# Optimization experiments

Measured on AMD Instinct MI355X. Metric: run time of the kernel, lower is better.

The kernel has to match this reference:

```python
import jax, jax.numpy as jnp
import numpy as np

B, T, D_IN, D_H, D_P = 256, 512, 256, 512, 512

def _lin(k, out_d, in_d):
    # torch nn.Linear default init: U(-1/sqrt(in_d), 1/sqrt(in_d))
    k1, k2 = jax.random.split(k)
    bound = 1.0 / np.sqrt(in_d)
    W = jax.random.uniform(k1, (out_d, in_d), jnp.float32, -bound, bound)
    b = jax.random.uniform(k2, (out_d,), jnp.float32, -bound, bound)
    return W, b

def setup_inputs() -> dict:
    key = jax.random.key(0)
    ks = jax.random.split(key, 8)
    x = jax.random.normal(ks[0], (B, T, D_IN), jnp.float32)
    # RNNCell params (torch init: U(-1/sqrt(hidden), 1/sqrt(hidden)) for all)
    bh = 1.0 / np.sqrt(D_H)
    k = jax.random.split(ks[1], 4)
    W_ih = jax.random.uniform(k[0], (D_H, D_IN), jnp.float32, -bh, bh)
    b_ih = jax.random.uniform(k[1], (D_H,), jnp.float32, -bh, bh)
    W_hh = jax.random.uniform(k[2], (D_H, D_H), jnp.float32, -bh, bh)
    b_hh = jax.random.uniform(k[3], (D_H,), jnp.float32, -bh, bh)
    W_ip, b_ip = _lin(ks[2], D_P, D_IN)
    W_hp, b_hp = _lin(ks[3], D_P, D_H)
    W_g, b_g = _lin(ks[4], D_P, D_IN + D_H)
    W_r, b_r = _lin(ks[5], D_P, D_P)
    W_o, b_o = _lin(ks[6], D_P, D_P)
    return dict(x=x, W_ih=W_ih, b_ih=b_ih, W_hh=W_hh, b_hh=b_hh,
                W_ip=W_ip, b_ip=b_ip, W_hp=W_hp, b_hp=b_hp,
                W_g=W_g, b_g=b_g, W_r=W_r, b_r=b_r, W_o=W_o, b_o=b_o)

def reference(x, W_ih, b_ih, W_hh, b_hh, W_ip, b_ip, W_hp, b_hp,
              W_g, b_g, W_r, b_r, W_o, b_o):
    batch = x.shape[0]
    # Precompute time-parallel projections of x outside the recurrence.
    x_ih = jnp.einsum('bti,hi->bth', x, W_ih) + b_ih + b_hh   # RNN input term
    x_proj_all = jnp.einsum('bti,pi->btp', x, W_ip) + b_ip
    # gate = sigmoid([x_t, h] @ W_g^T + b_g); split W_g into x-part and h-part
    W_gx, W_gh = W_g[:, :x.shape[-1]], W_g[:, x.shape[-1]:]
    gate_x_all = jnp.einsum('bti,pi->btp', x, W_gx) + b_g

    h0 = jnp.zeros((batch, W_hh.shape[0]), x.dtype)

    def step(h, inputs):
        x_ih_t, x_proj, gate_x = inputs
        h = jnp.tanh(x_ih_t + h @ W_hh.T)                # RNNCell (b_ih+b_hh folded in)
        h_proj = h @ W_hp.T + b_hp
        gate = jax.nn.sigmoid(gate_x + h @ W_gh.T)
        blended = gate * h_proj + (1.0 - gate) * x_proj
        res = blended @ W_r.T + b_r
        out_t = jax.nn.relu(res + blended)
        out_t = out_t @ W_o.T + b_o
        return h, out_t

    xs = (jnp.swapaxes(x_ih, 0, 1),       # (T, B, H)
          jnp.swapaxes(x_proj_all, 0, 1), # (T, B, P)
          jnp.swapaxes(gate_x_all, 0, 1)) # (T, B, P)
    _, outs = jax.lax.scan(step, h0, xs)
    return jnp.swapaxes(outs, 0, 1)       # (B, T, P)
```

## Files before the change

kernel.cpp:

```cpp
#include <hip/hip_runtime.h>
#include <hip/hip_bf16.h>
#include <cstdint>

#define RB   256
#define RT   512
#define ROWS (RB*RT)

typedef __attribute__((ext_vector_type(8))) short bf16x8;
typedef __attribute__((ext_vector_type(4))) short s16x4;
typedef __attribute__((ext_vector_type(4))) float f32x4;

#define DEV static __device__ __forceinline__

DEV float bf2f(unsigned short u){
  union { unsigned int i; float f; } v; v.i = ((unsigned int)u) << 16; return v.f;
}
DEV float blo(unsigned int u){
  union { unsigned int i; float f; } v; v.i = u << 16; return v.f;
}
DEV float bhi(unsigned int u){
  union { unsigned int i; float f; } v; v.i = u & 0xffff0000u; return v.f;
}
DEV unsigned short f2bf(float f){
  union { float f; unsigned int i; } v; v.f = f;
  unsigned int x = v.i;
  return (unsigned short)((x + 0x7fffu + ((x >> 16) & 1u)) >> 16);
}
DEV unsigned int cvt_pk_bf16(float lo, float hi){
  unsigned int r;
  asm("v_cvt_pk_bf16_f32 %0, %1, %2" : "=v"(r) : "v"(lo), "v"(hi));
  return r;
}
DEV float tanh_fast(float x){
  float e  = __expf(2.f * x);
  return 1.f - 2.f * __builtin_amdgcn_rcpf(e + 1.f);
}
DEV float sigmoid_fast(float x){
  float xc = fminf(fmaxf(x, -30.f), 30.f);
  return __builtin_amdgcn_rcpf(1.f + __expf(-xc));
}
DEV void gl_lds16(const void* g, void* l){
  __builtin_amdgcn_global_load_lds(
      (const __attribute__((address_space(1))) unsigned int*)g,
      (__attribute__((address_space(3))) unsigned int*)l, 16, 0, 0);
}

struct ConvArgs {
  const float* src[15];
  unsigned short* dst[15];
  long pre[16];
};

__global__ __launch_bounds__(256) void conv_k(ConvArgs a, long total)
{
  long stride = (long)gridDim.x * blockDim.x;
  for (long idx = (long)blockIdx.x * blockDim.x + threadIdx.x; idx < total; idx += stride){
    int t = 0;
    #pragma unroll
    for (int j = 0; j < 14; j++) t += (idx >= a.pre[j + 1]) ? 1 : 0;
    long local = idx - a.pre[t];
    float4 v = ((const float4*)a.src[t])[local];
    s16x4 o;
    o[0] = (short)f2bf(v.x); o[1] = (short)f2bf(v.y);
    o[2] = (short)f2bf(v.z); o[3] = (short)f2bf(v.w);
    ((s16x4*)a.dst[t])[local] = o;
  }
}

__global__ __launch_bounds__(256, 2) void gemm_k(
    const unsigned short* __restrict__ A, int lda,
    const unsigned short* __restrict__ W, int ldb,
    const unsigned short* __restrict__ bias,
    const unsigned short* __restrict__ bias2,
    const unsigned short* __restrict__ addsrc,
    void* __restrict__ C,
    int K, int act, int out_f32)
{
  __shared__ unsigned short As[128*64];
  __shared__ unsigned short Bs[128*64];
  const int tid = threadIdx.x, w = tid >> 6, l = tid & 63;
  const int wm = w >> 1, wn = w & 1;
  const int lr = l & 15, lk = (l >> 4) * 8;
  const long row0 = (long)blockIdx.x * 128;
  const int  col0 = blockIdx.y * 128;

  f32x4 acc[4][4] = {};

  for (int k0 = 0; k0 < K; k0 += 64){
    __syncthreads();
    #pragma unroll
    for (int i = 0; i < 4; i++){
      int chunk = i*256 + tid;
      int r = chunk >> 3, kc = (chunk & 7) * 8;
      gl_lds16(A + (row0 + r)*lda + k0 + kc, (unsigned short*)As + (i*256 + w*64)*8);
      gl_lds16(W + (long)(col0 + r)*ldb + k0 + kc, (unsigned short*)Bs + (i*256 + w*64)*8);
    }
    asm volatile("s_waitcnt vmcnt(0)" ::: "memory");
    __syncthreads();
    #pragma unroll
    for (int ks = 0; ks < 2; ks++){
      bf16x8 a[4], b[4];
      #pragma unroll
      for (int mt = 0; mt < 4; mt++) a[mt] = *(const bf16x8*)&As[(wm*64 + mt*16 + lr)*64 + ks*32 + lk];
      #pragma unroll
      for (int nt = 0; nt < 4; nt++) b[nt] = *(const bf16x8*)&Bs[(wn*64 + nt*16 + lr)*64 + ks*32 + lk];
      #pragma unroll
      for (int mt = 0; mt < 4; mt++)
        #pragma unroll
        for (int nt = 0; nt < 4; nt++)
          acc[mt][nt] = __builtin_amdgcn_mfma_f32_16x16x32_bf16(a[mt], b[nt], acc[mt][nt], 0, 0, 0);
    }
  }

  #pragma unroll
  for (int nt = 0; nt < 4; nt++){
    int c = col0 + wn*64 + nt*16 + lr;
    float bv = bf2f(bias[c]);
    if (bias2) bv += bf2f(bias2[c]);
    #pragma unroll
    for (int mt = 0; mt < 4; mt++){
      #pragma unroll
      for (int i = 0; i < 4; i++){
        long r = row0 + wm*64 + mt*16 + (l >> 4)*4 + i;
        float v = acc[mt][nt][i] + bv;
        if (addsrc) v += bf2f(addsrc[r*512 + c]);
        if (act) v = fmaxf(v, 0.f);
        if (out_f32) ((float*)C)[r*512 + c] = v;
        else ((unsigned short*)C)[r*512 + c] = f2bf(v);
      }
    }
  }
}

__global__ __launch_bounds__(512, 2) void recur_k(
    const unsigned short* __restrict__ xih,
    const unsigned short* __restrict__ Whh,
    unsigned short* __restrict__ H)
{
  extern __shared__ unsigned short lds[];
  unsigned short* Wl = lds;
  unsigned short* hb = lds + 512*136;

  const int tid = threadIdx.x, w = tid >> 6, l = tid & 63;
  const int lr = l & 15, hi = l >> 4, lk = hi * 8;
  const int b0 = blockIdx.x * 16;
  const int cbase = w * 64;

  #pragma unroll
  for (int i = 0; i < 16; i++){
    int id = i*512 + tid;
    int c = id >> 4, j = (id & 15) * 8;
    *(bf16x8*)&Wl[c*136 + j] = *(const bf16x8*)&Whh[c*512 + 384 + j];
  }
  for (int i = tid; i < 16*520; i += 512) hb[i] = 0;

  bf16x8 wa[4][12];
  #pragma unroll
  for (int nt = 0; nt < 4; nt++){
    const unsigned short* wp = Whh + (cbase + nt*16 + lr)*512 + lk;
    #pragma unroll
    for (int ks = 0; ks < 12; ks++)
      wa[nt][ks] = *(const bf16x8*)&wp[ks*32];
  }
  #pragma unroll
  for (int nt = 0; nt < 4; nt++)
    #pragma unroll
    for (int ks = 0; ks < 12; ks++)
      asm volatile("" : "+v"(wa[nt][ks]));

  __syncthreads();

  const unsigned short* hrd = &hb[lr*520 + lk];
  const unsigned short* wlb = &Wl[(cbase + lr)*136 + lk];
  unsigned short*       hwr = &hb[lr*520 + cbase + hi*4];

  const long xbase = ((long)(b0 + lr) * RT) * 512 + cbase + hi*4;
  const unsigned short* xr = xih + xbase;
  unsigned short*       hr = H   + xbase;

  #pragma unroll 1
  for (int t = 0; t < RT; t++){
    uint2 xu[4];
    #pragma unroll
    for (int nt = 0; nt < 4; nt++)
      xu[nt] = *(const uint2*)(xr + nt*16);

    f32x4 acc[4] = {};
    #pragma unroll
    for (int ks = 0; ks < 12; ks++){
      bf16x8 hf = *(const bf16x8*)(hrd + ks*32);
      #pragma unroll
      for (int nt = 0; nt < 4; nt++)
        acc[nt] = __builtin_amdgcn_mfma_f32_16x16x32_bf16(wa[nt][ks], hf, acc[nt], 0, 0, 0);
    }
    #pragma unroll
    for (int ks = 0; ks < 4; ks++){
      bf16x8 hf = *(const bf16x8*)(hrd + (12 + ks)*32);
      #pragma unroll
      for (int nt = 0; nt < 4; nt++){
        bf16x8 af = *(const bf16x8*)(wlb + (nt*16)*136 + ks*32);
        acc[nt] = __builtin_amdgcn_mfma_f32_16x16x32_bf16(af, hf, acc[nt], 0, 0, 0);
      }
    }

    uint2 P[4];
    #pragma unroll
    for (int nt = 0; nt < 4; nt++){
      float v0 = tanh_fast(acc[nt][0] + blo(xu[nt].x));
      float v1 = tanh_fast(acc[nt][1] + bhi(xu[nt].x));
      float v2 = tanh_fast(acc[nt][2] + blo(xu[nt].y));
      float v3 = tanh_fast(acc[nt][3] + bhi(xu[nt].y));
      P[nt].x = cvt_pk_bf16(v0, v1);
      P[nt].y = cvt_pk_bf16(v2, v3);
    }

    #pragma unroll
    for (int nt = 0; nt < 4; nt++)
      *(uint2*)(hr + nt*16) = P[nt];

    __syncthreads();
    #pragma unroll
    for (int nt = 0; nt < 4; nt++)
      *(uint2*)(hwr + nt*16) = P[nt];
    __syncthreads();

    xr += 512; hr += 512;
  }
}

__global__ __launch_bounds__(256, 2) void blend_k(
    const unsigned short* __restrict__ X,
    const unsigned short* __restrict__ Hm,
    const unsigned short* __restrict__ Wg,
    const unsigned short* __restrict__ Wip,
    const unsigned short* __restrict__ Whp,
    const unsigned short* __restrict__ bg,
    const unsigned short* __restrict__ bip,
    const unsigned short* __restrict__ bhp,
    unsigned short* __restrict__ Out)
{
  __shared__ unsigned short As[128*64];
  __shared__ unsigned short Gs[128*64];
  __shared__ unsigned short Ps[128*64];
  const int tid = threadIdx.x, w = tid >> 6, l = tid & 63;
  const int wm = w >> 1, wn = w & 1;
  const int lr = l & 15, lk = (l >> 4) * 8;
  const long row0 = (long)blockIdx.x * 128;
  const int  col0 = blockIdx.y * 128;

  f32x4 accg[4][4] = {}, accp[4][4] = {};
  unsigned int xpp[4][4][2];

  #pragma unroll 1
  for (int k0 = 0; k0 < 768; k0 += 64){
    const bool ph1 = (k0 < 256);
    __syncthreads();
    #pragma unroll
    for (int i = 0; i < 4; i++){
      int chunk = i*256 + tid;
      int r = chunk >> 3, kc = (chunk & 7) * 8;
      const unsigned short* asrc = ph1 ? (X  + (row0 + r)*256 + k0 + kc)
                                       : (Hm + (row0 + r)*512 + (k0 - 256) + kc);
      gl_lds16(asrc, (unsigned short*)As + (i*256 + w*64)*8);
      gl_lds16(Wg + (long)(col0 + r)*768 + k0 + kc, (unsigned short*)Gs + (i*256 + w*64)*8);
      const unsigned short* psrc = ph1 ? (Wip + (col0 + r)*256 + k0 + kc)
                                       : (Whp + (col0 + r)*512 + (k0 - 256) + kc);
      gl_lds16(psrc, (unsigned short*)Ps + (i*256 + w*64)*8);
    }
    asm volatile("s_waitcnt vmcnt(0)" ::: "memory");
    __syncthreads();
    #pragma unroll
    for (int ks = 0; ks < 2; ks++){
      bf16x8 a[4], gq[4], pq[4];
      #pragma unroll
      for (int mt = 0; mt < 4; mt++) a[mt]  = *(const bf16x8*)&As[(wm*64 + mt*16 + lr)*64 + ks*32 + lk];
      #pragma unroll
      for (int nt = 0; nt < 4; nt++){
        gq[nt] = *(const bf16x8*)&Gs[(wn*64 + nt*16 + lr)*64 + ks*32 + lk];
        pq[nt] = *(const bf16x8*)&Ps[(wn*64 + nt*16 + lr)*64 + ks*32 + lk];
      }
      #pragma unroll
      for (int mt = 0; mt < 4; mt++)
        #pragma unroll
        for (int nt = 0; nt < 4; nt++){
          accg[mt][nt] = __builtin_amdgcn_mfma_f32_16x16x32_bf16(a[mt], gq[nt], accg[mt][nt], 0, 0, 0);
          accp[mt][nt] = __builtin_amdgcn_mfma_f32_16x16x32_bf16(a[mt], pq[nt], accp[mt][nt], 0, 0, 0);
        }
    }
    if (k0 == 192){
      #pragma unroll
      for (int mt = 0; mt < 4; mt++)
        #pragma unroll
        for (int nt = 0; nt < 4; nt++){
          xpp[mt][nt][0] = (unsigned)f2bf(accp[mt][nt][0]) | ((unsigned)f2bf(accp[mt][nt][1]) << 16);
          xpp[mt][nt][1] = (unsigned)f2bf(accp[mt][nt][2]) | ((unsigned)f2bf(accp[mt][nt][3]) << 16);
          accp[mt][nt] = (f32x4){0.f, 0.f, 0.f, 0.f};
        }
    }
  }

  #pragma unroll
  for (int nt = 0; nt < 4; nt++){
    int c = col0 + wn*64 + nt*16 + lr;
    float bgv = bf2f(bg[c]), bipv = bf2f(bip[c]), bhpv = bf2f(bhp[c]);
    #pragma unroll
    for (int mt = 0; mt < 4; mt++){
      #pragma unroll
      for (int i = 0; i < 4; i++){
        long r = row0 + wm*64 + mt*16 + (l >> 4)*4 + i;
        float g  = sigmoid_fast(accg[mt][nt][i] + bgv);
        float hp = accp[mt][nt][i] + bhpv;
        unsigned u = xpp[mt][nt][i >> 1];
        float xp = bf2f((unsigned short)((i & 1) ? (u >> 16) : (u & 0xffff))) + bipv;
        float v = g * hp + (1.f - g) * xp;
        Out[r*512 + c] = f2bf(v);
      }
    }
  }
}

extern "C" void kernel_launch(void* const* d_in, const int* in_sizes, int n_in,
                              void* d_out, int out_size, void* d_ws, size_t ws_size,
                              hipStream_t stream)
{
  static const long nelem[15] = {
    (long)ROWS*256,
    512*256, 512,
    512*512, 512,
    512*256, 512,
    512*512, 512,
    512*768, 512,
    512*512, 512,
    512*512, 512
  };

  unsigned char* ob = (unsigned char*)d_out;
  unsigned char* wb = (unsigned char*)d_ws;
  ConvArgs ca;
  long pre = 0;
  size_t doff = 0;
  for (int i = 0; i < 15; i++){
    ca.src[i] = (const float*)d_in[i];
    if (i == 13)      ca.dst[i] = (unsigned short*)(wb + 134217728u);
    else if (i == 14) ca.dst[i] = (unsigned short*)(wb + 134742016u);
    else              ca.dst[i] = (unsigned short*)(ob + doff);
    ca.pre[i] = pre;
    pre += nelem[i] / 4;
    if (i == 0) doff = 67108864u;
    else if (i < 13) doff += (size_t)nelem[i] * 2;
  }
  ca.pre[15] = pre;
  const long total_chunks = pre;

  const unsigned short* xb  = ca.dst[0];
  const unsigned short* Wih = ca.dst[1];
  const unsigned short* bih = ca.dst[2];
  const unsigned short* Whh = ca.dst[3];
  const unsigned short* bhh = ca.dst[4];
  const unsigned short* Wip = ca.dst[5];
  const unsigned short* bip = ca.dst[6];
  const unsigned short* Whp = ca.dst[7];
  const unsigned short* bhp = ca.dst[8];
  const unsigned short* Wg  = ca.dst[9];
  const unsigned short* bg  = ca.dst[10];
  const unsigned short* Wr  = ca.dst[11];
  const unsigned short* br  = ca.dst[12];
  const unsigned short* Wo  = ca.dst[13];
  const unsigned short* bo  = ca.dst[14];

  unsigned short* xih  = (unsigned short*)(ob + 75497472u);
  unsigned short* wsb  = (unsigned short*)d_ws;

  dim3 grid(ROWS / 128, 4), block(256);

  conv_k<<<2048, 256, 0, stream>>>(ca, total_chunks);

  gemm_k<<<grid, block, 0, stream>>>(xb, 256, Wih, 256, bih, bhh, nullptr, xih, 256, 0, 0);

  static const int kRecurLds = 512*136*2 + 16*520*2;
  hipFuncSetAttribute((const void*)recur_k, hipFuncAttributeMaxDynamicSharedMemorySize, kRecurLds);
  recur_k<<<16, 512, kRecurLds, stream>>>(xih, Whh, wsb);

  blend_k<<<grid, block, 0, stream>>>(xb, wsb, Wg, Wip, Whp, bg, bip, bhp, xih);

  gemm_k<<<grid, block, 0, stream>>>(xih, 512, Wr, 512, br, nullptr, xih, wsb, 512, 1, 0);

  gemm_k<<<grid, block, 0, stream>>>(wsb, 512, Wo, 512, bo, nullptr, nullptr, d_out, 512, 0, 1);
}
```

Measured before the change: 2.103 ms.

## Double-buffer GEMM loads and restructure recurrence W_hh split across registers, LDS, global

```diff
diff --git a/kernel.cpp b/kernel.cpp
--- a/kernel.cpp
+++ b/kernel.cpp
@@ -9,6 +9,8 @@
 typedef __attribute__((ext_vector_type(8))) short bf16x8;
 typedef __attribute__((ext_vector_type(4))) short s16x4;
 typedef __attribute__((ext_vector_type(4))) float f32x4;
+typedef __attribute__((ext_vector_type(4))) int   i32x4;
+typedef unsigned long long ull;
 
 #define DEV static __device__ __forceinline__
 
@@ -65,6 +67,17 @@
     o[2] = (short)f2bf(v.z); o[3] = (short)f2bf(v.w);
     ((s16x4*)a.dst[t])[local] = o;
   }
+}
+
+__global__ __launch_bounds__(256) void wtail_k(
+    const unsigned short* __restrict__ Whh, unsigned short* __restrict__ Wt)
+{
+  int id = blockIdx.x * 256 + threadIdx.x;
+  int fi = id >> 6, l = id & 63;
+  int w  = fi >> 4, si = (fi >> 2) & 3, nt = fi & 3;
+  int row = w*64 + nt*16 + (l & 15);
+  int col = (12 + si)*32 + (l >> 4)*8;
+  *(bf16x8*)&Wt[(long)id * 8] = *(const bf16x8*)&Whh[row*512 + col];
 }
 
 __global__ __launch_bounds__(256, 2) void gemm_k(
@@ -76,8 +89,8 @@
     void* __restrict__ C,
     int K, int act, int out_f32)
 {
-  __shared__ unsigned short As[128*64];
-  __shared__ unsigned short Bs[128*64];
+  __shared__ unsigned short As[2][128*64];
+  __shared__ unsigned short Bs[2][128*64];
   const int tid = threadIdx.x, w = tid >> 6, l = tid & 63;
   const int wm = w >> 1, wn = w & 1;
   const int lr = l & 15, lk = (l >> 4) * 8;
@@ -86,31 +99,45 @@
 
   f32x4 acc[4][4] = {};
 
-  for (int k0 = 0; k0 < K; k0 += 64){
-    __syncthreads();
-    #pragma unroll
-    for (int i = 0; i < 4; i++){
-      int chunk = i*256 + tid;
-      int r = chunk >> 3, kc = (chunk & 7) * 8;
-      gl_lds16(A + (row0 + r)*lda + k0 + kc, (unsigned short*)As + (i*256 + w*64)*8);
-      gl_lds16(W + (long)(col0 + r)*ldb + k0 + kc, (unsigned short*)Bs + (i*256 + w*64)*8);
-    }
-    asm volatile("s_waitcnt vmcnt(0)" ::: "memory");
-    __syncthreads();
+#define GSTAGE(buf, kk) { \
+    _Pragma("unroll") \
+    for (int i = 0; i < 4; i++){ \
+      int chunk = i*256 + tid; \
+      int r = chunk >> 3, kc = (chunk & 7) * 8; \
+      gl_lds16(A + (row0 + r)*lda + (kk) + kc, (unsigned short*)As[buf] + (i*256 + w*64)*8); \
+      gl_lds16(W + (long)(col0 + r)*ldb + (kk) + kc, (unsigned short*)Bs[buf] + (i*256 + w*64)*8); \
+    } }
+
+  GSTAGE(0, 0)
+  const int nst = K >> 6;
+  for (int s = 0; s < nst; s++){
+    const int cb = s & 1;
+    if (s + 1 < nst){
+      GSTAGE(cb ^ 1, (s + 1) * 64)
+      asm volatile("s_waitcnt vmcnt(8)" ::: "memory");
+    } else {
+      asm volatile("s_waitcnt vmcnt(0)" ::: "memory");
+    }
+    __builtin_amdgcn_s_barrier();
+    asm volatile("" ::: "memory");
     #pragma unroll
     for (int ks = 0; ks < 2; ks++){
       bf16x8 a[4], b[4];
       #pragma unroll
-      for (int mt = 0; mt < 4; mt++) a[mt] = *(const bf16x8*)&As[(wm*64 + mt*16 + lr)*64 + ks*32 + lk];
-      #pragma unroll
-      for (int nt = 0; nt < 4; nt++) b[nt] = *(const bf16x8*)&Bs[(wn*64 + nt*16 + lr)*64 + ks*32 + lk];
+      for (int mt = 0; mt < 4; mt++) a[mt] = *(const bf16x8*)&As[cb][(wm*64 + mt*16 + lr)*64 + ks*32 + lk];
+      #pragma unroll
+      for (int nt = 0; nt < 4; nt++) b[nt] = *(const bf16x8*)&Bs[cb][(wn*64 + nt*16 + lr)*64 + ks*32 + lk];
       #pragma unroll
       for (int mt = 0; mt < 4; mt++)
         #pragma unroll
         for (int nt = 0; nt < 4; nt++)
           acc[mt][nt] = __builtin_amdgcn_mfma_f32_16x16x32_bf16(a[mt], b[nt], acc[mt][nt], 0, 0, 0);
     }
-  }
+    asm volatile("s_waitcnt lgkmcnt(0)" ::: "memory");
+    __builtin_amdgcn_s_barrier();
+    asm volatile("" ::: "memory");
+  }
+#undef GSTAGE
 
   #pragma unroll
   for (int nt = 0; nt < 4; nt++){
@@ -135,72 +162,104 @@
 __global__ __launch_bounds__(512, 2) void recur_k(
     const unsigned short* __restrict__ xih,
     const unsigned short* __restrict__ Whh,
+    const unsigned short* __restrict__ Wt,
     unsigned short* __restrict__ H)
 {
   extern __shared__ unsigned short lds[];
   unsigned short* Wl = lds;
-  unsigned short* hb = lds + 512*136;
+  unsigned short* hx = lds + 65536;
 
   const int tid = threadIdx.x, w = tid >> 6, l = tid & 63;
-  const int lr = l & 15, hi = l >> 4, lk = hi * 8;
+  const int lr = l & 15, hi = l >> 4;
   const int b0 = blockIdx.x * 16;
   const int cbase = w * 64;
 
   #pragma unroll
   for (int i = 0; i < 16; i++){
-    int id = i*512 + tid;
-    int c = id >> 4, j = (id & 15) * 8;
-    *(bf16x8*)&Wl[c*136 + j] = *(const bf16x8*)&Whh[c*512 + 384 + j];
-  }
-  for (int i = tid; i < 16*520; i += 512) hb[i] = 0;
-
-  bf16x8 wa[4][12];
+    int cid = i*512 + tid;
+    int fl = cid >> 6, ln = cid & 63;
+    int fw = fl >> 4, si = (fl >> 2) & 3, fnt = fl & 3;
+    int row = fw*64 + fnt*16 + (ln & 15);
+    int col = (8 + si)*32 + (ln >> 4)*8;
+    *(bf16x8*)&Wl[fl*512 + ln*8] = *(const bf16x8*)&Whh[row*512 + col];
+  }
+  {
+    ull* z = (ull*)hx;
+    for (int i = tid; i < 2048; i += 512) z[i] = 0;
+  }
+
+  bf16x8 wa[4][8];
   #pragma unroll
   for (int nt = 0; nt < 4; nt++){
-    const unsigned short* wp = Whh + (cbase + nt*16 + lr)*512 + lk;
-    #pragma unroll
-    for (int ks = 0; ks < 12; ks++)
+    const unsigned short* wp = Whh + (cbase + nt*16 + lr)*512 + hi*8;
+    #pragma unroll
+    for (int ks = 0; ks < 8; ks++)
       wa[nt][ks] = *(const bf16x8*)&wp[ks*32];
   }
   #pragma unroll
   for (int nt = 0; nt < 4; nt++)
     #pragma unroll
-    for (int ks = 0; ks < 12; ks++)
+    for (int ks = 0; ks < 8; ks++)
       asm volatile("" : "+v"(wa[nt][ks]));
 
   __syncthreads();
 
-  const unsigned short* hrd = &hb[lr*520 + lk];
-  const unsigned short* wlb = &Wl[(cbase + lr)*136 + lk];
-  unsigned short*       hwr = &hb[lr*520 + cbase + hi*4];
-
-  const long xbase = ((long)(b0 + lr) * RT) * 512 + cbase + hi*4;
-  const unsigned short* xr = xih + xbase;
-  unsigned short*       hr = H   + xbase;
+  const unsigned short* hrd = hx + l*8;
+  const unsigned short* wlb = Wl + (w*16)*512 + l*8;
+  const unsigned short* wtb = Wt + ((long)w*16*64 + l)*8;
+
+  const long xb = ((long)(b0 + lr) * RT) * 512 + cbase + hi*4;
+  const unsigned short* xr = xih + xb;
+  unsigned short*       hr = H   + xb;
+
+  unsigned short* hw0 = hx + (2*w    )*512;
+  unsigned short* hw1 = hx + (2*w + 1)*512;
+  const int so0 = (((hi >> 1)    )*16 + lr)*8 + (hi & 1)*4;
+  const int so1 = ((2 + (hi >> 1))*16 + lr)*8 + (hi & 1)*4;
+
+  uint2 xu[4];
+  #pragma unroll
+  for (int nt = 0; nt < 4; nt++) xu[nt] = *(const uint2*)(xr + nt*16);
 
   #pragma unroll 1
   for (int t = 0; t < RT; t++){
-    uint2 xu[4];
-    #pragma unroll
-    for (int nt = 0; nt < 4; nt++)
-      xu[nt] = *(const uint2*)(xr + nt*16);
+    bf16x8 s1[8];
+    #pragma unroll
+    for (int j = 0; j < 8; j++) s1[j] = *(const bf16x8*)(wtb + j*512);
 
     f32x4 acc[4] = {};
     #pragma unroll
-    for (int ks = 0; ks < 12; ks++){
-      bf16x8 hf = *(const bf16x8*)(hrd + ks*32);
+    for (int ks = 0; ks < 8; ks++){
+      bf16x8 hf = *(const bf16x8*)(hrd + ks*512);
       #pragma unroll
       for (int nt = 0; nt < 4; nt++)
         acc[nt] = __builtin_amdgcn_mfma_f32_16x16x32_bf16(wa[nt][ks], hf, acc[nt], 0, 0, 0);
     }
     #pragma unroll
-    for (int ks = 0; ks < 4; ks++){
-      bf16x8 hf = *(const bf16x8*)(hrd + (12 + ks)*32);
+    for (int si = 0; si < 4; si++){
+      bf16x8 hf = *(const bf16x8*)(hrd + (8 + si)*512);
       #pragma unroll
       for (int nt = 0; nt < 4; nt++){
-        bf16x8 af = *(const bf16x8*)(wlb + (nt*16)*136 + ks*32);
+        bf16x8 af = *(const bf16x8*)(wlb + (si*4 + nt)*512);
         acc[nt] = __builtin_amdgcn_mfma_f32_16x16x32_bf16(af, hf, acc[nt], 0, 0, 0);
       }
+    }
+    #pragma unroll
+    for (int si = 0; si < 2; si++){
+      bf16x8 hf = *(const bf16x8*)(hrd + (12 + si)*512);
+      #pragma unroll
+      for (int nt = 0; nt < 4; nt++)
+        acc[nt] = __builtin_amdgcn_mfma_f32_16x16x32_bf16(s1[si*4 + nt], hf, acc[nt], 0, 0, 0);
+    }
+    bf16x8 s2[8];
+    #pragma unroll
+    for (int j = 0; j < 8; j++) s2[j] = *(const bf16x8*)(wtb + (8 + j)*512);
+    #pragma unroll
+    for (int si = 0; si < 2; si++){
+      bf16x8 hf = *(const bf16x8*)(hrd + (14 + si)*512);
+      #pragma unroll
+      for (int nt = 0; nt < 4; nt++)
+        acc[nt] = __builtin_amdgcn_mfma_f32_16x16x32_bf16(s2[si*4 + nt], hf, acc[nt], 0, 0, 0);
     }
 
     uint2 P[4];
@@ -214,17 +273,28 @@
       P[nt].y = cvt_pk_bf16(v2, v3);
     }
 
+    if (t + 1 < RT){
+      #pragma unroll
+      for (int nt = 0; nt < 4; nt++) xu[nt] = *(const uint2*)(xr + 512 + nt*16);
+    }
+    xr += 512;
+
+    asm volatile("s_waitcnt lgkmcnt(0)" ::: "memory");
+    __builtin_amdgcn_s_barrier();
+    asm volatile("" ::: "memory");
+
+    *(uint2*)(hw0 + so0) = P[0];
+    *(uint2*)(hw0 + so1) = P[1];
+    *(uint2*)(hw1 + so0) = P[2];
+    *(uint2*)(hw1 + so1) = P[3];
     #pragma unroll
     for (int nt = 0; nt < 4; nt++)
       *(uint2*)(hr + nt*16) = P[nt];
-
-    __syncthreads();
-    #pragma unroll
-    for (int nt = 0; nt < 4; nt++)
-      *(uint2*)(hwr + nt*16) = P[nt];
-    __syncthreads();
-
-    xr += 512; hr += 512;
+    hr += 512;
+
+    asm volatile("s_waitcnt lgkmcnt(0)" ::: "memory");
+    __builtin_amdgcn_s_barrier();
+    asm volatile("" ::: "memory");
   }
 }
 
@@ -369,17 +439,20 @@
   const unsigned short* bo  = ca.dst[14];
 
   unsigned short* xih  = (unsigned short*)(ob + 75497472u);
+  unsigned short* Wtl  = (unsigned short*)(ob + 209715200u);
   unsigned short* wsb  = (unsigned short*)d_ws;
 
   dim3 grid(ROWS / 128, 4), block(256);
 
   conv_k<<<2048, 256, 0, stream>>>(ca, total_chunks);
 
+  wtail_k<<<32, 256, 0, stream>>>(Whh, Wtl);
+
   gemm_k<<<grid, block, 0, stream>>>(xb, 256, Wih, 256, bih, bhh, nullptr, xih, 256, 0, 0);
 
-  static const int kRecurLds = 512*136*2 + 16*520*2;
-  hipFuncSetAttribute((const void*)recur_k, hipFuncAttributeMaxDynamicSharedMemorySize, kRecurLds);
-  recur_k<<<16, 512, kRecurLds, stream>>>(xih, Whh, wsb);
+  static const int kRecurLds = 128*1024 + 16*1024;
+  (void)hipFuncSetAttribute((const void*)recur_k, hipFuncAttributeMaxDynamicSharedMemorySize, kRecurLds);
+  recur_k<<<16, 512, kRecurLds, stream>>>(xih, Whh, Wtl, wsb);
 
   blend_k<<<grid, block, 0, stream>>>(xb, wsb, Wg, Wip, Whp, bg, bip, bhp, xih);
 
```

After: 2.313 ms. 10.0% more time.
